# Kernel tuning notes

Measured on AMD Instinct MI355X. Metric: run time of the kernel, lower is better.

Reference implementation:

```python
import jax, jax.numpy as jnp
import numpy as np

N_NODES = 50000
N_EDGES = 800000
HIDDEN = 256          # hidden_size == output_size (same `inputs` feeds all projections)
NUM_HEADS = 8
D_K = HIDDEN // NUM_HEADS  # 32
SCALE = float(np.sqrt(D_K))


def setup_inputs() -> dict:
    key = jax.random.key(0)
    ks = jax.random.split(key, 8)
    w_std = 1.0 / np.sqrt(HIDDEN)
    inputs = jax.random.normal(ks[0], (N_NODES, HIDDEN), jnp.float32)
    src = jax.random.randint(ks[1], (N_EDGES,), 0, N_NODES, dtype=jnp.int32)
    # guarantee every node has >= 1 in-edge (avoid 0/0 in normalization)
    dst_rand = jax.random.randint(ks[2], (N_EDGES - N_NODES,), 0, N_NODES, dtype=jnp.int32)
    dst = jnp.concatenate([jnp.arange(N_NODES, dtype=jnp.int32), dst_rand])
    Wq = jax.random.normal(ks[3], (HIDDEN, HIDDEN), jnp.float32) * w_std
    bq = jnp.zeros((HIDDEN,), jnp.float32)
    Wk = jax.random.normal(ks[4], (HIDDEN, HIDDEN), jnp.float32) * w_std
    Wv = jax.random.normal(ks[5], (HIDDEN, HIDDEN), jnp.float32) * w_std
    Wo = jax.random.normal(ks[6], (HIDDEN, HIDDEN), jnp.float32) * w_std
    bo = jnp.zeros((HIDDEN,), jnp.float32)
    return {"inputs": inputs, "Wq": Wq, "bq": bq, "Wk": Wk, "Wv": Wv,
            "Wo": Wo, "bo": bo, "src": src, "dst": dst}


def reference(inputs, Wq, bq, Wk, Wv, Wo, bo, src, dst):
    n = inputs.shape[0]
    # projections (dropout is identity in eval mode)
    q = (inputs @ Wq.T + bq).reshape(n, NUM_HEADS, D_K)
    k = (inputs @ Wk.T).reshape(n, NUM_HEADS, D_K)
    v = (inputs @ Wv.T).reshape(n, NUM_HEADS, D_K)
    # edge-wise dot product score: k[src] . q[dst]  -> [E, H]
    score = jnp.einsum('ehd,ehd->eh', k[src], q[dst])
    score = jnp.exp(jnp.clip(score / SCALE, -10.0, 10.0))
    # weighted segment-sum aggregation over in-edges of each dst node
    wv = jax.ops.segment_sum(v[src] * score[..., None], dst, num_segments=n)  # [N,H,dk]
    z = jax.ops.segment_sum(score, dst, num_segments=n)                        # [N,H]
    o = (wv / z[..., None]).reshape(n, HIDDEN)
    return o @ Wo.T + bo
```

## Files before the change

### kernel.cpp

```cpp
#include <hip/hip_runtime.h>
#include <hip/hip_bf16.h>
#include <math.h>

#define HIDDEN 256
#define INV_SCALE 0.17677669529663687f

typedef __attribute__((ext_vector_type(8))) short short8;
typedef __attribute__((ext_vector_type(4))) float f32x4;
typedef const __attribute__((address_space(1))) unsigned int* gas_ptr;
typedef __attribute__((address_space(3))) unsigned int* las_ptr;

static __device__ __forceinline__ unsigned short f2bf(float x) {
  unsigned u = __float_as_uint(x);
  unsigned r = (u + 0x7FFF + ((u >> 16) & 1)) >> 16;
  return (unsigned short)r;
}
static __device__ __forceinline__ float bf2f(unsigned short u) {
  return __uint_as_float((unsigned)u << 16);
}

#define GLL(gp, lp) __builtin_amdgcn_global_load_lds((gas_ptr)(const void*)(gp), (las_ptr)(void*)(lp), 16, 0, 0)


__global__ __launch_bounds__(256) void conv_a_kernel(const float* __restrict__ in,
                                                     unsigned short* __restrict__ out,
                                                     int total4) {
  int stride = gridDim.x * blockDim.x;
  for (int i = blockIdx.x * blockDim.x + threadIdx.x; i < total4; i += stride) {
    float4 f = ((const float4*)in)[i];
    ushort4 u;
    u.x = f2bf(f.x); u.y = f2bf(f.y); u.z = f2bf(f.z); u.w = f2bf(f.w);
    ((ushort4*)out)[i] = u;
  }
}

__global__ __launch_bounds__(256) void conv_w_kernel(const float* __restrict__ Wq,
                                                     const float* __restrict__ Wk,
                                                     const float* __restrict__ Wv,
                                                     const float* __restrict__ Wo,
                                                     unsigned short* __restrict__ wqkv,
                                                     unsigned short* __restrict__ wob) {
  int i = blockIdx.x * 256 + threadIdx.x;
  int m = i >> 16;
  int j = i & 65535;
  const float* s = (m == 0) ? Wq : (m == 1) ? Wk : (m == 2) ? Wv : Wo;
  unsigned short b = f2bf(s[j]);
  if (m < 3) wqkv[m * 65536 + j] = b;
  else wob[j] = b;
}


__global__ __launch_bounds__(256) void hist_kernel(const int* __restrict__ dst,
                                                   int* __restrict__ deg, int E) {
  int e = blockIdx.x * blockDim.x + threadIdx.x;
  if (e < E) atomicAdd(&deg[dst[e]], 1);
}

__global__ __launch_bounds__(256) void scan1_kernel(const int* __restrict__ deg,
                                                    int* __restrict__ offs,
                                                    int* __restrict__ bsums, int N) {
  __shared__ int s[256];
  int tid = threadIdx.x;
  int base = blockIdx.x * 1024 + tid * 4;
  int v0 = (base + 0 < N) ? deg[base + 0] : 0;
  int v1 = (base + 1 < N) ? deg[base + 1] : 0;
  int v2 = (base + 2 < N) ? deg[base + 2] : 0;
  int v3 = (base + 3 < N) ? deg[base + 3] : 0;
  int tsum = v0 + v1 + v2 + v3;
  s[tid] = tsum;
  __syncthreads();
  for (int off = 1; off < 256; off <<= 1) {
    int t = (tid >= off) ? s[tid - off] : 0;
    __syncthreads();
    s[tid] += t;
    __syncthreads();
  }
  int excl = s[tid] - tsum;
  if (base + 0 < N) offs[base + 0] = excl;
  if (base + 1 < N) offs[base + 1] = excl + v0;
  if (base + 2 < N) offs[base + 2] = excl + v0 + v1;
  if (base + 3 < N) offs[base + 3] = excl + v0 + v1 + v2;
  if (tid == 255) bsums[blockIdx.x] = s[255];
}

__global__ void scan2_kernel(int* __restrict__ bsums, int nb) {
  if (blockIdx.x == 0 && threadIdx.x == 0) {
    int run = 0;
    for (int b = 0; b < nb; ++b) { int t = bsums[b]; bsums[b] = run; run += t; }
  }
}

__global__ __launch_bounds__(256) void scan3_kernel(int* __restrict__ offs,
                                                    int* __restrict__ cursor,
                                                    const int* __restrict__ bsums,
                                                    int N, int E) {
  int i = blockIdx.x * blockDim.x + threadIdx.x;
  if (i < N) {
    int v = offs[i] + bsums[i >> 10];
    offs[i] = v;
    cursor[i] = v;
  }
  if (i == 0) offs[N] = E;
}

__global__ __launch_bounds__(256) void scatter_kernel(const int* __restrict__ dst,
                                                      const int* __restrict__ src,
                                                      int* __restrict__ cursor,
                                                      int* __restrict__ esrc, int E) {
  int e = blockIdx.x * blockDim.x + threadIdx.x;
  if (e < E) {
    int n = dst[e];
    int pos = atomicAdd(&cursor[n], 1);
    esrc[pos] = src[e];
  }
}

template <int MODE>
__global__ __launch_bounds__(256) void gemm_alds(const unsigned short* __restrict__ A,
                                                 const unsigned short* __restrict__ B,
                                                 const float* __restrict__ bias,
                                                 float* __restrict__ Cf,
                                                 unsigned short* __restrict__ Cq,
                                                 unsigned short* __restrict__ Ck,
                                                 unsigned short* __restrict__ Cv,
                                                 int M) {
  constexpr int NT = (MODE == 0) ? 6 : 2;
  constexpr int NU = NT * 8;
  __shared__ unsigned short As[8][128][32];
  __shared__ unsigned short Bs[2][128][32];
  int tid = threadIdx.x;
  int lane = tid & 63;
  int wid = tid >> 6;
  int wm = wid >> 1, wn = wid & 1;
  int brow = blockIdx.x * 128;
  int fr = lane & 15;
  int kg = (lane >> 4) * 8;

  int srow = wid * 32 + (lane >> 2);
  int skoff = (lane & 3) * 8;

  const unsigned short* gA = &A[(size_t)(brow + srow) * HIDDEN + skoff];
#pragma unroll
  for (int kk = 0; kk < 8; ++kk) {
    char* dA = (char*)&As[kk][0][0] + wid * 2048;
    GLL(gA + kk * 32, dA);
    GLL(gA + kk * 32 + 16 * HIDDEN, dA + 1024);
  }

  const unsigned short* gBbase = &B[(size_t)srow * HIDDEN + skoff];
  auto stageB = [&](int u) {
    int ct = u >> 3, kk = u & 7;
    const unsigned short* gB = gBbase + (size_t)(ct * 128) * HIDDEN + kk * 32;
    char* dB = (char*)&Bs[u & 1][0][0] + wid * 2048;
    GLL(gB, dB);
    GLL(gB + 16 * HIDDEN, dB + 1024);
  };

  f32x4 acc[4][4];
#pragma unroll
  for (int mi = 0; mi < 4; ++mi)
#pragma unroll
    for (int ni = 0; ni < 4; ++ni) acc[mi][ni] = (f32x4){0.f, 0.f, 0.f, 0.f};

  stageB(0);

  for (int u = 0; u < NU; ++u) {
    int kk = u & 7;
    if (u + 1 < NU) {
      stageB(u + 1);
      asm volatile("s_waitcnt vmcnt(2)" ::: "memory");
    } else {
      asm volatile("s_waitcnt vmcnt(0)" ::: "memory");
    }
    __builtin_amdgcn_s_barrier();
    __builtin_amdgcn_sched_barrier(0);
    short8 af[4], bf4[4];
#pragma unroll
    for (int mi = 0; mi < 4; ++mi)
      af[mi] = *(const short8*)&As[kk][wm * 64 + mi * 16 + fr][kg];
#pragma unroll
    for (int ni = 0; ni < 4; ++ni)
      bf4[ni] = *(const short8*)&Bs[u & 1][wn * 64 + ni * 16 + fr][kg];
#pragma unroll
    for (int mi = 0; mi < 4; ++mi)
#pragma unroll
      for (int ni = 0; ni < 4; ++ni)
        acc[mi][ni] = __builtin_amdgcn_mfma_f32_16x16x32_bf16(af[mi], bf4[ni], acc[mi][ni], 0, 0, 0);
    if (kk == 7) {
      int ct = u >> 3;
      int fq = lane >> 4;
#pragma unroll
      for (int mi = 0; mi < 4; ++mi) {
#pragma unroll
        for (int ni = 0; ni < 4; ++ni) {
          int c = ct * 128 + wn * 64 + ni * 16 + fr;
#pragma unroll
          for (int j = 0; j < 4; ++j) {
            int r = brow + wm * 64 + mi * 16 + fq * 4 + j;
            if (r < M) {
              float val = acc[mi][ni][j];
              if (MODE == 1) {
                Cf[(size_t)r * HIDDEN + c] = val + bias[c];
              } else {
                if (c < 256) Cq[(size_t)r * HIDDEN + c] = f2bf(val + bias[c]);
                else if (c < 512) Ck[(size_t)r * HIDDEN + (c - 256)] = f2bf(val);
                else Cv[(size_t)r * HIDDEN + (c - 512)] = f2bf(val);
              }
            }
          }
          acc[mi][ni] = (f32x4){0.f, 0.f, 0.f, 0.f};
        }
      }
    }
    __builtin_amdgcn_s_barrier();
  }
}

__global__ __launch_bounds__(256) void agg_kernel(const unsigned short* __restrict__ q,
                                                  const unsigned short* __restrict__ k,
                                                  const unsigned short* __restrict__ v,
                                                  const int* __restrict__ offs,
                                                  const int* __restrict__ esrc,
                                                  unsigned short* __restrict__ o, int N) {
  int n = blockIdx.x * 4 + (threadIdx.x >> 6);
  if (n >= N) return;
  int lane = threadIdx.x & 63;
  int half = lane >> 5;
  int l = lane & 31;

  float qf[8];
  {
    ushort4 qa = *(const ushort4*)&q[(size_t)n * HIDDEN + l * 8];
    ushort4 qb = *(const ushort4*)&q[(size_t)n * HIDDEN + l * 8 + 4];
    qf[0] = bf2f(qa.x); qf[1] = bf2f(qa.y); qf[2] = bf2f(qa.z); qf[3] = bf2f(qa.w);
    qf[4] = bf2f(qb.x); qf[5] = bf2f(qb.y); qf[6] = bf2f(qb.z); qf[7] = bf2f(qb.w);
  }

  int e0 = offs[n], e1 = offs[n + 1];
  float wv[8] = {};
  float z = 0.f;

  for (int idx = e0; idx < e1; idx += 2) {
    int my = idx + half;
    bool valid = my < e1;
    int s = esrc[valid ? my : idx];
    const ushort4* kp = (const ushort4*)&k[(size_t)s * HIDDEN + l * 8];
    const ushort4* vp = (const ushort4*)&v[(size_t)s * HIDDEN + l * 8];
    ushort4 ka = kp[0], kb = kp[1];
    ushort4 va = vp[0], vb = vp[1];
    float dot = qf[0] * bf2f(ka.x) + qf[1] * bf2f(ka.y) + qf[2] * bf2f(ka.z) + qf[3] * bf2f(ka.w)
              + qf[4] * bf2f(kb.x) + qf[5] * bf2f(kb.y) + qf[6] * bf2f(kb.z) + qf[7] * bf2f(kb.w);
    dot += __shfl_xor(dot, 1);
    dot += __shfl_xor(dot, 2);
    float e = 0.f;
    if (valid) e = __expf(fminf(fmaxf(dot * INV_SCALE, -10.f), 10.f));
    wv[0] += e * bf2f(va.x); wv[1] += e * bf2f(va.y);
    wv[2] += e * bf2f(va.z); wv[3] += e * bf2f(va.w);
    wv[4] += e * bf2f(vb.x); wv[5] += e * bf2f(vb.y);
    wv[6] += e * bf2f(vb.z); wv[7] += e * bf2f(vb.w);
    z += e;
  }

#pragma unroll
  for (int j = 0; j < 8; ++j) wv[j] += __shfl_xor(wv[j], 32);
  z += __shfl_xor(z, 32);

  if (half == 0) {
    float inv = 1.0f / z;
    ushort4 o0, o1;
    o0.x = f2bf(wv[0] * inv); o0.y = f2bf(wv[1] * inv);
    o0.z = f2bf(wv[2] * inv); o0.w = f2bf(wv[3] * inv);
    o1.x = f2bf(wv[4] * inv); o1.y = f2bf(wv[5] * inv);
    o1.z = f2bf(wv[6] * inv); o1.w = f2bf(wv[7] * inv);
    ushort4* op = (ushort4*)&o[(size_t)n * HIDDEN + l * 8];
    op[0] = o0; op[1] = o1;
  }
}


extern "C" void kernel_launch(void* const* d_in, const int* in_sizes, int n_in,
                              void* d_out, int out_size, void* d_ws, size_t ws_size,
                              hipStream_t stream) {
  const float* inputs = (const float*)d_in[0];
  const float* Wq = (const float*)d_in[1];
  const float* bq = (const float*)d_in[2];
  const float* Wk = (const float*)d_in[3];
  const float* Wv = (const float*)d_in[4];
  const float* Wo = (const float*)d_in[5];
  const float* bo = (const float*)d_in[6];
  const int* src = (const int*)d_in[7];
  const int* dst = (const int*)d_in[8];

  int N = in_sizes[0] / HIDDEN;
  int E = in_sizes[7];
  int Mpad = N + 128;

  char* w = (char*)d_ws;
  unsigned short* a_bf = (unsigned short*)w; w += (size_t)Mpad * HIDDEN * 2;
  unsigned short* qb = (unsigned short*)w;   w += (size_t)N * HIDDEN * 2;
  unsigned short* kb = (unsigned short*)w;   w += (size_t)N * HIDDEN * 2;
  unsigned short* vb = (unsigned short*)w;   w += (size_t)N * HIDDEN * 2;
  unsigned short* ob = (unsigned short*)w;   w += (size_t)Mpad * HIDDEN * 2;
  unsigned short* wqkv = (unsigned short*)w; w += (size_t)768 * HIDDEN * 2;
  unsigned short* wob = (unsigned short*)w;  w += (size_t)256 * HIDDEN * 2;
  int* deg = (int*)w;    w += (size_t)N * 4;
  int* offs = (int*)w;   w += (size_t)(N + 4) * 4;
  int* cursor = (int*)w; w += (size_t)N * 4;
  int* esrc = (int*)w;   w += (size_t)E * 4;
  int* bsums = (int*)w;  w += 256 * 4;

  conv_a_kernel<<<2048, 256, 0, stream>>>(inputs, a_bf, N * (HIDDEN / 4));
  conv_w_kernel<<<1024, 256, 0, stream>>>(Wq, Wk, Wv, Wo, wqkv, wob);

  hipMemsetAsync(deg, 0, (size_t)N * 4, stream);
  int eb = (E + 255) / 256;
  hist_kernel<<<eb, 256, 0, stream>>>(dst, deg, E);
  int nb = (N + 1023) / 1024;
  scan1_kernel<<<nb, 256, 0, stream>>>(deg, offs, bsums, N);
  scan2_kernel<<<1, 64, 0, stream>>>(bsums, nb);
  scan3_kernel<<<(N + 255) / 256, 256, 0, stream>>>(offs, cursor, bsums, N, E);
  scatter_kernel<<<eb, 256, 0, stream>>>(dst, src, cursor, esrc, E);

  int gblocks = (N + 127) / 128;
  gemm_alds<0><<<gblocks, 256, 0, stream>>>(a_bf, wqkv, bq, nullptr, qb, kb, vb, N);

  agg_kernel<<<(N + 3) / 4, 256, 0, stream>>>(qb, kb, vb, offs, esrc, ob, N);

  gemm_alds<1><<<gblocks, 256, 0, stream>>>(ob, wob, bo, (float*)d_out, nullptr, nullptr, nullptr, N);
}
```

Measured before the change: 338.4 us.

## Fuse fp32-to-bf16 input conversion into QKV GEMM and shrink row tile to 64

```diff
diff --git a/kernel.cpp b/kernel.cpp
--- a/kernel.cpp
+++ b/kernel.cpp
@@ -20,19 +20,6 @@
 }
 
 #define GLL(gp, lp) __builtin_amdgcn_global_load_lds((gas_ptr)(const void*)(gp), (las_ptr)(void*)(lp), 16, 0, 0)
-
-
-__global__ __launch_bounds__(256) void conv_a_kernel(const float* __restrict__ in,
-                                                     unsigned short* __restrict__ out,
-                                                     int total4) {
-  int stride = gridDim.x * blockDim.x;
-  for (int i = blockIdx.x * blockDim.x + threadIdx.x; i < total4; i += stride) {
-    float4 f = ((const float4*)in)[i];
-    ushort4 u;
-    u.x = f2bf(f.x); u.y = f2bf(f.y); u.z = f2bf(f.z); u.w = f2bf(f.w);
-    ((ushort4*)out)[i] = u;
-  }
-}
 
 __global__ __launch_bounds__(256) void conv_w_kernel(const float* __restrict__ Wq,
                                                      const float* __restrict__ Wk,
@@ -116,37 +103,28 @@
 }
 
 template <int MODE>
-__global__ __launch_bounds__(256) void gemm_alds(const unsigned short* __restrict__ A,
-                                                 const unsigned short* __restrict__ B,
-                                                 const float* __restrict__ bias,
-                                                 float* __restrict__ Cf,
-                                                 unsigned short* __restrict__ Cq,
-                                                 unsigned short* __restrict__ Ck,
-                                                 unsigned short* __restrict__ Cv,
-                                                 int M) {
+__global__ __launch_bounds__(256) void gemm_alds64(const void* __restrict__ Araw,
+                                                   const unsigned short* __restrict__ B,
+                                                   const float* __restrict__ bias,
+                                                   float* __restrict__ Cf,
+                                                   unsigned short* __restrict__ Cq,
+                                                   unsigned short* __restrict__ Ck,
+                                                   unsigned short* __restrict__ Cv,
+                                                   int M) {
   constexpr int NT = (MODE == 0) ? 6 : 2;
   constexpr int NU = NT * 8;
-  __shared__ unsigned short As[8][128][32];
+  __shared__ unsigned short As[8][64][32];
   __shared__ unsigned short Bs[2][128][32];
   int tid = threadIdx.x;
   int lane = tid & 63;
   int wid = tid >> 6;
   int wm = wid >> 1, wn = wid & 1;
-  int brow = blockIdx.x * 128;
+  int brow = blockIdx.x * 64;
   int fr = lane & 15;
   int kg = (lane >> 4) * 8;
 
   int srow = wid * 32 + (lane >> 2);
   int skoff = (lane & 3) * 8;
-
-  const unsigned short* gA = &A[(size_t)(brow + srow) * HIDDEN + skoff];
-#pragma unroll
-  for (int kk = 0; kk < 8; ++kk) {
-    char* dA = (char*)&As[kk][0][0] + wid * 2048;
-    GLL(gA + kk * 32, dA);
-    GLL(gA + kk * 32 + 16 * HIDDEN, dA + 1024);
-  }
-
   const unsigned short* gBbase = &B[(size_t)srow * HIDDEN + skoff];
   auto stageB = [&](int u) {
     int ct = u >> 3, kk = u & 7;
@@ -156,13 +134,41 @@
     GLL(gB + 16 * HIDDEN, dB + 1024);
   };
 
-  f32x4 acc[4][4];
-#pragma unroll
-  for (int mi = 0; mi < 4; ++mi)
+  stageB(0);
+
+  if (MODE == 0) {
+    const float* A = (const float*)Araw;
+#pragma unroll
+    for (int p = 0; p < 16; ++p) {
+      int i4 = p * 256 + tid;
+      int row = i4 >> 6;
+      int c4 = i4 & 63;
+      int col = c4 * 4;
+      int grow = brow + row; if (grow >= M) grow = M - 1;
+      float4 f = *(const float4*)&A[(size_t)grow * HIDDEN + col];
+      ushort4 u4;
+      u4.x = f2bf(f.x); u4.y = f2bf(f.y); u4.z = f2bf(f.z); u4.w = f2bf(f.w);
+      *(ushort4*)&As[col >> 5][row][col & 31] = u4;
+    }
+  } else {
+    const unsigned short* A = (const unsigned short*)Araw;
+#pragma unroll
+    for (int p = 0; p < 8; ++p) {
+      int i8 = p * 256 + tid;
+      int row = i8 >> 5;
+      int c8 = i8 & 31;
+      int col = c8 * 8;
+      short8 s8 = *(const short8*)&A[(size_t)(brow + row) * HIDDEN + col];
+      *(short8*)&As[col >> 5][row][col & 31] = s8;
+    }
+  }
+  __syncthreads();
+
+  f32x4 acc[2][4];
+#pragma unroll
+  for (int mi = 0; mi < 2; ++mi)
 #pragma unroll
     for (int ni = 0; ni < 4; ++ni) acc[mi][ni] = (f32x4){0.f, 0.f, 0.f, 0.f};
-
-  stageB(0);
 
   for (int u = 0; u < NU; ++u) {
     int kk = u & 7;
@@ -174,15 +180,15 @@
     }
     __builtin_amdgcn_s_barrier();
     __builtin_amdgcn_sched_barrier(0);
-    short8 af[4], bf4[4];
-#pragma unroll
-    for (int mi = 0; mi < 4; ++mi)
-      af[mi] = *(const short8*)&As[kk][wm * 64 + mi * 16 + fr][kg];
+    short8 af[2], bf4[4];
+#pragma unroll
+    for (int mi = 0; mi < 2; ++mi)
+      af[mi] = *(const short8*)&As[kk][wm * 32 + mi * 16 + fr][kg];
 #pragma unroll
     for (int ni = 0; ni < 4; ++ni)
       bf4[ni] = *(const short8*)&Bs[u & 1][wn * 64 + ni * 16 + fr][kg];
 #pragma unroll
-    for (int mi = 0; mi < 4; ++mi)
+    for (int mi = 0; mi < 2; ++mi)
 #pragma unroll
       for (int ni = 0; ni < 4; ++ni)
         acc[mi][ni] = __builtin_amdgcn_mfma_f32_16x16x32_bf16(af[mi], bf4[ni], acc[mi][ni], 0, 0, 0);
@@ -190,13 +196,13 @@
       int ct = u >> 3;
       int fq = lane >> 4;
 #pragma unroll
-      for (int mi = 0; mi < 4; ++mi) {
+      for (int mi = 0; mi < 2; ++mi) {
 #pragma unroll
         for (int ni = 0; ni < 4; ++ni) {
           int c = ct * 128 + wn * 64 + ni * 16 + fr;
 #pragma unroll
           for (int j = 0; j < 4; ++j) {
-            int r = brow + wm * 64 + mi * 16 + fq * 4 + j;
+            int r = brow + wm * 32 + mi * 16 + fq * 4 + j;
             if (r < M) {
               float val = acc[mi][ni][j];
               if (MODE == 1) {
@@ -296,7 +302,6 @@
   int Mpad = N + 128;
 
   char* w = (char*)d_ws;
-  unsigned short* a_bf = (unsigned short*)w; w += (size_t)Mpad * HIDDEN * 2;
   unsigned short* qb = (unsigned short*)w;   w += (size_t)N * HIDDEN * 2;
   unsigned short* kb = (unsigned short*)w;   w += (size_t)N * HIDDEN * 2;
   unsigned short* vb = (unsigned short*)w;   w += (size_t)N * HIDDEN * 2;
@@ -309,7 +314,6 @@
   int* esrc = (int*)w;   w += (size_t)E * 4;
   int* bsums = (int*)w;  w += 256 * 4;
 
-  conv_a_kernel<<<2048, 256, 0, stream>>>(inputs, a_bf, N * (HIDDEN / 4));
   conv_w_kernel<<<1024, 256, 0, stream>>>(Wq, Wk, Wv, Wo, wqkv, wob);
 
   hipMemsetAsync(deg, 0, (size_t)N * 4, stream);
@@ -321,10 +325,10 @@
   scan3_kernel<<<(N + 255) / 256, 256, 0, stream>>>(offs, cursor, bsums, N, E);
   scatter_kernel<<<eb, 256, 0, stream>>>(dst, src, cursor, esrc, E);
 
-  int gblocks = (N + 127) / 128;
-  gemm_alds<0><<<gblocks, 256, 0, stream>>>(a_bf, wqkv, bq, nullptr, qb, kb, vb, N);
+  int gblocks = (N + 63) / 64;
+  gemm_alds64<0><<<gblocks, 256, 0, stream>>>(inputs, wqkv, bq, nullptr, qb, kb, vb, N);
 
   agg_kernel<<<(N + 3) / 4, 256, 0, stream>>>(qb, kb, vb, offs, esrc, ob, N);
 
-  gemm_alds<1><<<gblocks, 256, 0, stream>>>(ob, wob, bo, (float*)d_out, nullptr, nullptr, nullptr, N);
-}
+  gemm_alds64<1><<<gblocks, 256, 0, stream>>>(ob, wob, bo, (float*)d_out, nullptr, nullptr, nullptr, N);
+}
```

Result: no change. 340.1 us (+0.5%).
